# Optimization experiments

Measured on AMD Instinct MI355X. Metric: run time of the kernel, lower is better.

The kernel has to match this reference:

```python
import jax, jax.numpy as jnp
import numpy as np

S = 1024   # query_len == key_len (self-attention)
B = 4      # batch
E = 1024   # embed_dim
H = 16     # num_heads
D = E // H # head_dim = 64
PE = 2 * S # positional table rows


def setup_inputs() -> dict:
    rng = jax.random.key(0)
    ks = jax.random.split(rng, 12)
    f = lambda k, sh, s: jax.random.normal(k, sh, dtype=jnp.float32) * s
    W = 0.02  # weight scale (xavier-ish for E=1024)
    return {
        'query': f(ks[0], (S, B, E), 1.0),
        'key': f(ks[1], (S, B, E), 1.0),
        'value': f(ks[2], (S, B, E), 1.0),
        'pe': f(ks[3], (PE, E), 1.0),
        'w_q': f(ks[4], (E, E), W),
        'w_k': f(ks[5], (E, E), W),
        'w_v': f(ks[6], (E, E), W),
        'w_k_pos': f(ks[7], (E, E), W),
        'content_bias': f(ks[8], (H, D), 0.02),
        'pos_bias': f(ks[9], (H, D), 0.02),
        'w_out': f(ks[10], (E, E), W),
        'b_out': f(ks[11], (E,), 0.02),
    }


def _rel_shift(pos):
    # pos: [B, H, Q, M] with M = 2*K - 1. Transformer-XL pad/narrow shift trick.
    Bn, h, Q, M = pos.shape
    p = jnp.pad(pos, ((0, 0), (0, 0), (0, 1), (0, 1)))          # [B,H,Q+1,M+1]
    p = p.reshape(Bn, h, (Q + 1) * (M + 1))
    p = p[:, :, M // 2: M // 2 + M * Q].reshape(Bn, h, Q, M)
    return p[..., :(M + 1) // 2]                                 # [B,H,Q,K]


def reference(query, key, value, pe, w_q, w_k, w_v, w_k_pos,
              content_bias, pos_bias, w_out, b_out):
    Q, Bn, Em = query.shape
    K = key.shape[0]
    h, d = content_bias.shape
    scaling = d ** -0.5

    # projections (nn.Linear: x @ W.T), split heads -> [B,H,len,d]
    q = (query @ w_q.T).reshape(Q, Bn, h, d).transpose(1, 2, 0, 3)
    k = (key   @ w_k.T).reshape(K, Bn, h, d).transpose(1, 2, 0, 3)
    v = (value @ w_v.T).reshape(K, Bn, h, d).transpose(1, 2, 0, 3)

    # relative position keys: centered slice of pe table, size 2K-1
    M = 2 * K - 1
    lower = pe.shape[0] // 2 - K + 1  # offset = 0
    k_pos = (pe[lower:lower + M] @ w_k_pos.T).reshape(M, h, d).transpose(1, 0, 2)  # [H,M,d]

    content = jnp.einsum('bhqd,bhkd->bhqk', q + content_bias[None, :, None, :], k)
    pos = jnp.einsum('bhqd,hmd->bhqm', q + pos_bias[None, :, None, :], k_pos)
    pos = _rel_shift(pos)  # [B,H,Q,K]

    attn = jax.nn.softmax((content + pos) * scaling, axis=-1)
    out = jnp.einsum('bhqk,bhkd->bhqd', attn, v)        # [B,H,Q,d]
    out = out.transpose(2, 0, 1, 3).reshape(Q, Bn, Em)  # [Q,B,E]
    return out @ w_out.T + b_out
```

## Files before the change

### kernel.cpp

```cpp
#include <hip/hip_runtime.h>


typedef short s16x8 __attribute__((ext_vector_type(8)));
typedef __bf16 bf16x8 __attribute__((ext_vector_type(8)));
typedef float f32x4 __attribute__((ext_vector_type(4)));
typedef unsigned int u32;

__device__ __forceinline__ float b2f(short s) {
  u32 u = ((u32)(unsigned short)s) << 16;
  return __builtin_bit_cast(float, u);
}
__device__ __forceinline__ short f2b(float f) {
  u32 u = __builtin_bit_cast(u32, f);
  u32 r = u + 0x7FFFu + ((u >> 16) & 1u);
  return (short)(r >> 16);
}

__device__ __forceinline__ f32x4 mfma_bf16(s16x8 a, s16x8 b, f32x4 c) {
  return __builtin_amdgcn_mfma_f32_16x16x32_bf16(
      __builtin_bit_cast(bf16x8, a), __builtin_bit_cast(bf16x8, b), c, 0, 0, 0);
}

__device__ __forceinline__ void glds16(void* l, const void* g) {
  __builtin_amdgcn_global_load_lds(
      (const __attribute__((address_space(1))) void*)g,
      (__attribute__((address_space(3))) void*)l, 16, 0, 0);
}

__global__ __launch_bounds__(256) void cvt_all(
    const float* __restrict__ q, const float* __restrict__ k,
    const float* __restrict__ v, const float* __restrict__ pe,
    const float* __restrict__ wq, const float* __restrict__ wk,
    const float* __restrict__ wv, const float* __restrict__ wkp,
    const float* __restrict__ wo, short* __restrict__ dst)
{
  const int c = blockIdx.x * 256 + threadIdx.x;
  int idx = c * 8;
  const float* src;
  if      (idx < 4194304)  { src = q; }
  else if (idx < 8388608)  { src = k;   idx -= 4194304; }
  else if (idx < 12582912) { src = v;   idx -= 8388608; }
  else if (idx < 14680064) { src = pe;  idx -= 12582912; }
  else if (idx < 15728640) { src = wq;  idx -= 14680064; }
  else if (idx < 16777216) { src = wk;  idx -= 15728640; }
  else if (idx < 17825792) { src = wv;  idx -= 16777216; }
  else if (idx < 18874368) { src = wkp; idx -= 17825792; }
  else                     { src = wo;  idx -= 18874368; }
  float4 x = *(const float4*)(src + idx);
  float4 y = *(const float4*)(src + idx + 4);
  s16x8 o;
  o[0] = f2b(x.x); o[1] = f2b(x.y); o[2] = f2b(x.z); o[3] = f2b(x.w);
  o[4] = f2b(y.x); o[5] = f2b(y.y); o[6] = f2b(y.z); o[7] = f2b(y.w);
  *(s16x8*)(dst + (long)c * 8) = o;
}

__device__ __forceinline__ void gemm_core_bf16(
    const short* __restrict__ A, const short* __restrict__ W,
    short* At, short* Wt, f32x4 (&acc)[4][4], int bm, int bn)
{
  const int t = threadIdx.x;
  const int lane = t & 63, w = t >> 6;
  const int wm = w >> 1, wn = w & 1;
  const int quad = lane >> 4, lo16 = lane & 15;
  const int srow = t >> 2;
  const int skc = (t & 3) * 8;
  const int soff = t * 16;

  const short* Ag0 = A + (bm * 128 + srow) * 1024 + skc;
  const short* Wg0 = W + (bn * 128 + srow) * 1024 + skc;
  char* AtB = (char*)At;
  char* WtB = (char*)Wt;

  for (int k0 = 0; k0 < 1024; k0 += 32) {
    glds16(AtB + soff,        Ag0 + k0);
    glds16(AtB + 4096 + soff, Ag0 + 64 * 1024 + k0);
    glds16(WtB + soff,        Wg0 + k0);
    glds16(WtB + 4096 + soff, Wg0 + 64 * 1024 + k0);
    __syncthreads();
    s16x8 af[4], bfr[4];
#pragma unroll
    for (int mt = 0; mt < 4; ++mt)
      af[mt] = *(const s16x8*)(At + (wm * 64 + mt * 16 + lo16) * 32 + quad * 8);
#pragma unroll
    for (int nt = 0; nt < 4; ++nt)
      bfr[nt] = *(const s16x8*)(Wt + (wn * 64 + nt * 16 + lo16) * 32 + quad * 8);
#pragma unroll
    for (int mt = 0; mt < 4; ++mt)
#pragma unroll
      for (int nt = 0; nt < 4; ++nt)
        acc[mt][nt] = mfma_bf16(af[mt], bfr[nt], acc[mt][nt]);
    __syncthreads();
  }
}

__global__ __launch_bounds__(256) void proj_gemm(
    const short* __restrict__ qsrc, const short* __restrict__ ksrc,
    const short* __restrict__ vsrc, const short* __restrict__ pesrc,
    const short* __restrict__ wqb, const short* __restrict__ wkb,
    const short* __restrict__ wvb, const short* __restrict__ wkpb,
    short* __restrict__ qo, short* __restrict__ ko,
    short* __restrict__ vo, short* __restrict__ po)
{
  const int z = blockIdx.z;
  const short* A; const short* W; int M;
  if (z == 0)      { A = qsrc;  W = wqb;  M = 4096; }
  else if (z == 1) { A = ksrc;  W = wkb;  M = 4096; }
  else if (z == 2) { A = vsrc;  W = wvb;  M = 4096; }
  else             { A = pesrc; W = wkpb; M = 2048; }
  const int bm = blockIdx.x, bn = blockIdx.y;
  if (bm * 128 >= M) return;

  __shared__ __align__(16) short At[128 * 32];
  __shared__ __align__(16) short Wt[128 * 32];
  f32x4 acc[4][4] = {};
  gemm_core_bf16(A, W, At, Wt, acc, bm, bn);

  const int t = threadIdx.x;
  const int lane = t & 63, w = t >> 6;
  const int wm = w >> 1, wn = w & 1;
  const int quad = lane >> 4, lo16 = lane & 15;
#pragma unroll
  for (int mt = 0; mt < 4; ++mt) {
#pragma unroll
    for (int nt = 0; nt < 4; ++nt) {
#pragma unroll
      for (int r = 0; r < 4; ++r) {
        int m = bm * 128 + wm * 64 + mt * 16 + quad * 4 + r;
        int n = bn * 128 + wn * 64 + nt * 16 + lo16;
        short val = f2b(acc[mt][nt][r]);
        if (z <= 1) {
          short* o = (z == 0) ? qo : ko;
          int s = m >> 2, b = m & 3, hh = n >> 6, d = n & 63;
          o[((b * 16 + hh) * 1024 + s) * 64 + d] = val;
        } else if (z == 2) {
          int s = m >> 2, b = m & 3, hh = n >> 6, d = n & 63;
          vo[((b * 16 + hh) * 64 + d) * 1024 + s] = val;
        } else {
          int hh = n >> 6, d = n & 63;
          po[(hh * 2048 + m) * 64 + d] = val;
        }
      }
    }
  }
}

__global__ __launch_bounds__(256) void out_gemm(
    const short* __restrict__ A, const short* __restrict__ W,
    const float* __restrict__ bias, float* __restrict__ out)
{
  const int bm = blockIdx.x, bn = blockIdx.y;
  __shared__ __align__(16) short At[128 * 32];
  __shared__ __align__(16) short Wt[128 * 32];
  f32x4 acc[4][4] = {};
  gemm_core_bf16(A, W, At, Wt, acc, bm, bn);

  const int t = threadIdx.x;
  const int lane = t & 63, w = t >> 6;
  const int wm = w >> 1, wn = w & 1;
  const int quad = lane >> 4, lo16 = lane & 15;
#pragma unroll
  for (int mt = 0; mt < 4; ++mt) {
#pragma unroll
    for (int nt = 0; nt < 4; ++nt) {
#pragma unroll
      for (int r = 0; r < 4; ++r) {
        int m = bm * 128 + wm * 64 + mt * 16 + quad * 4 + r;
        int n = bn * 128 + wn * 64 + nt * 16 + lo16;
        out[m * 1024 + n] = acc[mt][nt][r] + bias[n];
      }
    }
  }
}

__global__ __launch_bounds__(256) void attn_kernel(
    const short* __restrict__ qatt, const short* __restrict__ katt,
    const short* __restrict__ vT, const short* __restrict__ kpe,
    const float* __restrict__ cbias, const float* __restrict__ pbias,
    short* __restrict__ aout)
{
  const int q0 = blockIdx.x * 64;
  const int h = blockIdx.y;
  const int b = blockIdx.z;
  const int bh = b * 16 + h;
  const int t = threadIdx.x;
  const int w = t >> 6, lane = t & 63;
  const int quad = lane >> 4, lo16 = lane & 15;

  __shared__ __align__(16) short Kt[64][72];
  __shared__ __align__(16) short Vt[64][72];
  __shared__ __align__(16) short KP[128][72];
  __shared__ __align__(16) short Pt[4][16 * 72];
  __shared__ __align__(16) float Sf[4][16 * 84];
  short* Pt_w = Pt[w];
  float* Sf_w = Sf[w];

  s16x8 a_c[2], a_p[2];
  {
    const int qg = q0 + 16 * w + lo16;
    const short* qrow = qatt + (bh * 1024 + qg) * 64;
#pragma unroll
    for (int ds = 0; ds < 2; ++ds) {
      const int d0 = ds * 32 + quad * 8;
      s16x8 qv = *(const s16x8*)(qrow + d0);
#pragma unroll
      for (int j = 0; j < 8; ++j) {
        float qf = b2f(qv[j]);
        a_c[ds][j] = f2b(qf + cbias[h * 64 + d0 + j]);
        a_p[ds][j] = f2b(qf + pbias[h * 64 + d0 + j]);
      }
    }
  }

  f32x4 O[4] = {};
  float lrow[4] = {0.f, 0.f, 0.f, 0.f};

  const int ro = 48 - 16 * w;

  for (int kt = 0; kt < 16; ++kt) {
    const int k0 = kt * 64;
    __syncthreads();
    {
      const int r = t >> 2, c = (t & 3) * 16;
      const s16x8* gk = (const s16x8*)(katt + (bh * 1024 + k0 + r) * 64 + c);
      s16x8 ka = gk[0], kb2 = gk[1];
      const s16x8* gv = (const s16x8*)(vT + (bh * 64 + r) * 1024 + k0 + c);
      s16x8 va = gv[0], vb = gv[1];
      *(s16x8*)&Kt[r][c] = ka;  *(s16x8*)&Kt[r][c + 8] = kb2;
      *(s16x8*)&Vt[r][c] = va;  *(s16x8*)&Vt[r][c + 8] = vb;
    }
    {
      const int i = t >> 1, c0 = (t & 1) * 32;
      int j = 960 + k0 - q0 + i;
      if (j > 2046) j = 2046;
      const s16x8* g = (const s16x8*)(kpe + (h * 2048 + j + 1) * 64 + c0);
      s16x8 x0 = g[0], x1 = g[1], x2 = g[2], x3 = g[3];
      *(s16x8*)&KP[i][c0] = x0;      *(s16x8*)&KP[i][c0 + 8] = x1;
      *(s16x8*)&KP[i][c0 + 16] = x2; *(s16x8*)&KP[i][c0 + 24] = x3;
    }
    __syncthreads();

    f32x4 sc[4];
#pragma unroll
    for (int nt = 0; nt < 4; ++nt) {
      f32x4 a = {0.f, 0.f, 0.f, 0.f};
#pragma unroll
      for (int ds = 0; ds < 2; ++ds) {
        s16x8 bf = *(const s16x8*)(&Kt[nt * 16 + lo16][ds * 32 + quad * 8]);
        a = mfma_bf16(a_c[ds], bf, a);
      }
      sc[nt] = a;
    }
    f32x4 sp[5];
#pragma unroll
    for (int nt = 0; nt < 5; ++nt) {
      f32x4 a = {0.f, 0.f, 0.f, 0.f};
#pragma unroll
      for (int ds = 0; ds < 2; ++ds) {
        s16x8 bf = *(const s16x8*)(&KP[ro + nt * 16 + lo16][ds * 32 + quad * 8]);
        a = mfma_bf16(a_p[ds], bf, a);
      }
      sp[nt] = a;
    }

#pragma unroll
    for (int nt = 0; nt < 5; ++nt)
#pragma unroll
      for (int r = 0; r < 4; ++r)
        Sf_w[(quad * 4 + r) * 84 + nt * 16 + lo16] = sp[nt][r];
    __builtin_amdgcn_wave_barrier();
    float s[4][4];
#pragma unroll
    for (int nt = 0; nt < 4; ++nt)
#pragma unroll
      for (int r = 0; r < 4; ++r) {
        int qi = quad * 4 + r;
        int ki = nt * 16 + lo16;
        float pos = Sf_w[qi * 84 + ki + 15 - qi];
        s[nt][r] = (sc[nt][r] + pos) * 0.125f;
      }
    __builtin_amdgcn_wave_barrier();

#pragma unroll
    for (int r = 0; r < 4; ++r) {
      short pb16[4];
#pragma unroll
      for (int nt = 0; nt < 4; ++nt) {
        float p = __expf(s[nt][r]);
        pb16[nt] = f2b(p);
        lrow[r] += b2f(pb16[nt]);
      }
#pragma unroll
      for (int nt = 0; nt < 4; ++nt)
        Pt_w[(quad * 4 + r) * 72 + nt * 16 + lo16] = pb16[nt];
    }
    __builtin_amdgcn_wave_barrier();

    s16x8 ap[2];
#pragma unroll
    for (int ks = 0; ks < 2; ++ks)
      ap[ks] = *(const s16x8*)(&Pt_w[lo16 * 72 + ks * 32 + quad * 8]);
    __builtin_amdgcn_wave_barrier();
#pragma unroll
    for (int ntd = 0; ntd < 4; ++ntd) {
#pragma unroll
      for (int ks = 0; ks < 2; ++ks) {
        s16x8 bv = *(const s16x8*)(&Vt[ntd * 16 + lo16][ks * 32 + quad * 8]);
        O[ntd] = mfma_bf16(ap[ks], bv, O[ntd]);
      }
    }
  }

#pragma unroll
  for (int r = 0; r < 4; ++r) {
#pragma unroll
    for (int off = 1; off < 16; off <<= 1)
      lrow[r] += __shfl_xor(lrow[r], off, 64);
    float rl = 1.f / lrow[r];
    int qg = q0 + 16 * w + quad * 4 + r;
#pragma unroll
    for (int ntd = 0; ntd < 4; ++ntd) {
      int d = ntd * 16 + lo16;
      aout[(qg * 4 + b) * 1024 + h * 64 + d] = f2b(O[ntd][r] * rl);
    }
  }
}

extern "C" void kernel_launch(void* const* d_in, const int* in_sizes, int n_in,
                              void* d_out, int out_size, void* d_ws, size_t ws_size,
                              hipStream_t stream) {
  (void)in_sizes; (void)n_in; (void)out_size; (void)ws_size;
  const float* query = (const float*)d_in[0];
  const float* key   = (const float*)d_in[1];
  const float* value = (const float*)d_in[2];
  const float* pe    = (const float*)d_in[3];
  const float* wq    = (const float*)d_in[4];
  const float* wk    = (const float*)d_in[5];
  const float* wv    = (const float*)d_in[6];
  const float* wkp   = (const float*)d_in[7];
  const float* cb    = (const float*)d_in[8];
  const float* pb    = (const float*)d_in[9];
  const float* wout  = (const float*)d_in[10];
  const float* bout  = (const float*)d_in[11];

  short* ws    = (short*)d_ws;
  short* qsrc  = ws;
  short* ksrc  = ws + 4194304;
  short* vsrc  = ws + 8388608;
  short* pesrc = ws + 12582912;
  short* wqb   = ws + 14680064;
  short* wkb   = ws + 15728640;
  short* wvb   = ws + 16777216;
  short* wkpb  = ws + 17825792;
  short* woutb = ws + 18874368;
  short* qatt  = ws + 19922944;
  short* katt  = ws + 24117248;
  short* vT    = ws + 28311552;
  short* kpe   = ws + 32505856;
  short* aout  = qsrc;

  cvt_all<<<dim3(9728), 256, 0, stream>>>(
      query, key, value, pe, wq, wk, wv, wkp, wout, ws);
  proj_gemm<<<dim3(32, 8, 4), 256, 0, stream>>>(
      qsrc, ksrc, vsrc, pesrc, wqb, wkb, wvb, wkpb, qatt, katt, vT, kpe);
  attn_kernel<<<dim3(16, 16, 4), 256, 0, stream>>>(
      qatt, katt, vT, kpe, cb, pb, aout);
  out_gemm<<<dim3(32, 8), 256, 0, stream>>>(aout, woutb, bout, (float*)d_out);
}
```

Baseline: 291.4 us.

## Load attention K, V and positional keys directly from global memory, dropping LDS staging

Removes the shared-memory tiles for K, V and positional keys and the two block-wide barriers per key tile. Each wave now reads its MFMA B operands straight from global memory through precomputed base pointers. It also adds an occupancy hint of 4 blocks per CU to launch_bounds. The aim is to cut LDS traffic and synchronization, at the cost of every wave fetching K and V redundantly from global memory or cache, plus more latency exposed on each MFMA operand load.

Measured after the change: 396.4 us. 1.36x slower.

```diff
diff --git a/kernel.cpp b/kernel.cpp
--- a/kernel.cpp
+++ b/kernel.cpp
@@ -172,7 +172,7 @@
   }
 }
 
-__global__ __launch_bounds__(256) void attn_kernel(
+__global__ __launch_bounds__(256, 4) void attn_kernel(
     const short* __restrict__ qatt, const short* __restrict__ katt,
     const short* __restrict__ vT, const short* __restrict__ kpe,
     const float* __restrict__ cbias, const float* __restrict__ pbias,
@@ -186,9 +186,6 @@
   const int w = t >> 6, lane = t & 63;
   const int quad = lane >> 4, lo16 = lane & 15;
 
-  __shared__ __align__(16) short Kt[64][72];
-  __shared__ __align__(16) short Vt[64][72];
-  __shared__ __align__(16) short KP[128][72];
   __shared__ __align__(16) short Pt[4][16 * 72];
   __shared__ __align__(16) float Sf[4][16 * 84];
   short* Pt_w = Pt[w];
@@ -216,28 +213,13 @@
 
   const int ro = 48 - 16 * w;
 
+  const short* kbase = katt + (bh * 1024 + lo16) * 64 + quad * 8;
+  const short* vbase = vT + (bh * 64 + lo16) * 1024 + quad * 8;
+  const int jb = 961 - q0 + ro + lo16;
+  const short* pbase = kpe + h * 2048 * 64 + quad * 8;
+
   for (int kt = 0; kt < 16; ++kt) {
     const int k0 = kt * 64;
-    __syncthreads();
-    {
-      const int r = t >> 2, c = (t & 3) * 16;
-      const s16x8* gk = (const s16x8*)(katt + (bh * 1024 + k0 + r) * 64 + c);
-      s16x8 ka = gk[0], kb2 = gk[1];
-      const s16x8* gv = (const s16x8*)(vT + (bh * 64 + r) * 1024 + k0 + c);
-      s16x8 va = gv[0], vb = gv[1];
-      *(s16x8*)&Kt[r][c] = ka;  *(s16x8*)&Kt[r][c + 8] = kb2;
-      *(s16x8*)&Vt[r][c] = va;  *(s16x8*)&Vt[r][c + 8] = vb;
-    }
-    {
-      const int i = t >> 1, c0 = (t & 1) * 32;
-      int j = 960 + k0 - q0 + i;
-      if (j > 2046) j = 2046;
-      const s16x8* g = (const s16x8*)(kpe + (h * 2048 + j + 1) * 64 + c0);
-      s16x8 x0 = g[0], x1 = g[1], x2 = g[2], x3 = g[3];
-      *(s16x8*)&KP[i][c0] = x0;      *(s16x8*)&KP[i][c0 + 8] = x1;
-      *(s16x8*)&KP[i][c0 + 16] = x2; *(s16x8*)&KP[i][c0 + 24] = x3;
-    }
-    __syncthreads();
 
     f32x4 sc[4];
 #pragma unroll
@@ -245,7 +227,7 @@
       f32x4 a = {0.f, 0.f, 0.f, 0.f};
 #pragma unroll
       for (int ds = 0; ds < 2; ++ds) {
-        s16x8 bf = *(const s16x8*)(&Kt[nt * 16 + lo16][ds * 32 + quad * 8]);
+        s16x8 bf = *(const s16x8*)(kbase + (k0 + nt * 16) * 64 + ds * 32);
         a = mfma_bf16(a_c[ds], bf, a);
       }
       sc[nt] = a;
@@ -253,10 +235,12 @@
     f32x4 sp[5];
 #pragma unroll
     for (int nt = 0; nt < 5; ++nt) {
+      int j = jb + k0 + nt * 16;
+      if (j > 2047) j = 2047;
       f32x4 a = {0.f, 0.f, 0.f, 0.f};
 #pragma unroll
       for (int ds = 0; ds < 2; ++ds) {
-        s16x8 bf = *(const s16x8*)(&KP[ro + nt * 16 + lo16][ds * 32 + quad * 8]);
+        s16x8 bf = *(const s16x8*)(pbase + j * 64 + ds * 32);
         a = mfma_bf16(a_p[ds], bf, a);
       }
       sp[nt] = a;
@@ -300,11 +284,12 @@
     for (int ks = 0; ks < 2; ++ks)
       ap[ks] = *(const s16x8*)(&Pt_w[lo16 * 72 + ks * 32 + quad * 8]);
     __builtin_amdgcn_wave_barrier();
+
 #pragma unroll
     for (int ntd = 0; ntd < 4; ++ntd) {
 #pragma unroll
       for (int ks = 0; ks < 2; ++ks) {
-        s16x8 bv = *(const s16x8*)(&Vt[ntd * 16 + lo16][ks * 32 + quad * 8]);
+        s16x8 bv = *(const s16x8*)(vbase + ntd * 16 * 1024 + k0 + ks * 32);
         O[ntd] = mfma_bf16(ap[ks], bv, O[ntd]);
       }
     }
```
